# Kernel tuning notes

Measured on AMD Instinct MI355X. Metric: run time of the kernel, lower is better.

Reference implementation:

```python
import jax, jax.numpy as jnp
import numpy as np

N_NODES = 50000
N_EDGES = 800000
NUM_GRAPHS = 512


def gcn_conv(x, edge_index, W, b, num_nodes):
    # PyG GCNConv: h = D^{-1/2} (A + I) D^{-1/2} (x @ W) + b
    h = x @ W
    src, dst = edge_index[0], edge_index[1]
    loop = jnp.arange(num_nodes)
    src = jnp.concatenate([src, loop])
    dst = jnp.concatenate([dst, loop])
    deg = jax.ops.segment_sum(jnp.ones_like(dst, dtype=h.dtype), dst,
                              num_segments=num_nodes)
    dinv = jnp.where(deg > 0, jax.lax.rsqrt(deg), 0.0)
    norm = dinv[src] * dinv[dst]                      # [E+N]
    msg = h[src] * norm[:, None]                      # gather + scale
    out = jax.ops.segment_sum(msg, dst, num_segments=num_nodes)  # scatter-add
    return out + b


def global_mean_pool(x, batch, num_graphs):
    sums = jax.ops.segment_sum(x, batch, num_segments=num_graphs)
    cnts = jax.ops.segment_sum(jnp.ones((x.shape[0],), x.dtype), batch,
                               num_segments=num_graphs)
    return sums / jnp.maximum(cnts, 1.0)[:, None]


def setup_inputs() -> dict:
    key = jax.random.key(0)
    ks = jax.random.split(key, 8)
    x = jax.random.normal(ks[0], (N_NODES, 128), dtype=jnp.float32)
    edge_index = jax.random.randint(ks[1], (2, N_EDGES), 0, N_NODES, dtype=jnp.int64)
    batch = jnp.sort(jax.random.randint(ks[2], (N_NODES,), 0, NUM_GRAPHS, dtype=jnp.int64))
    W1 = jax.random.normal(ks[3], (128, 128), dtype=jnp.float32) * (1.0 / np.sqrt(128))
    b1 = jnp.zeros((128,), jnp.float32)
    W2 = jax.random.normal(ks[4], (128, 64), dtype=jnp.float32) * (1.0 / np.sqrt(128))
    b2 = jnp.zeros((64,), jnp.float32)
    Wl = jax.random.normal(ks[5], (64, 64), dtype=jnp.float32) * (1.0 / np.sqrt(64))
    bl = jnp.zeros((64,), jnp.float32)
    return {"x": x, "edge_index": edge_index, "batch": batch,
            "W1": W1, "b1": b1, "W2": W2, "b2": b2, "Wl": Wl, "bl": bl}


def reference(x, edge_index, batch, W1, b1, W2, b2, Wl, bl):
    num_nodes = x.shape[0]
    h = gcn_conv(x, edge_index, W1, b1, num_nodes)
    h = jax.nn.relu(h)
    h = gcn_conv(h, edge_index, W2, b2, num_nodes)
    g = global_mean_pool(h, batch, NUM_GRAPHS)
    # dropout p=0.5 is identity in eval mode
    return g @ Wl + bl
```

## Files before the change

kernel.cpp:

```cpp
#include <hip/hip_runtime.h>
#include <hip/hip_fp16.h>
#include <math.h>


#define FEAT1 128
#define FEAT2 64
#define BCAP 8192


__global__ void binit_kernel(int* __restrict__ bucket_cursor, int nb) {
    int b = blockIdx.x * 256 + threadIdx.x;
    if (b < nb) bucket_cursor[b] = b * BCAP;
}

__global__ __launch_bounds__(256) void bin_scatter(const int* __restrict__ esrc,
                                                   const int* __restrict__ edst,
                                                   int ne, int nb,
                                                   int* __restrict__ bucket_cursor,
                                                   int* __restrict__ ebin) {
    __shared__ int lcnt[256];
    __shared__ int lcur[256];
    const int tid = threadIdx.x;
    const int e0 = blockIdx.x * 8192;
    lcnt[tid] = 0;
    __syncthreads();
    #pragma unroll 4
    for (int k = 0; k < 32; k++) {
        int e = e0 + k * 256 + tid;
        if (e < ne) atomicAdd(&lcnt[edst[e] >> 8], 1);
    }
    __syncthreads();
    if (tid < nb && lcnt[tid] > 0)
        lcur[tid] = atomicAdd(&bucket_cursor[tid], lcnt[tid]);
    __syncthreads();
    #pragma unroll 4
    for (int k = 0; k < 32; k++) {
        int e = e0 + k * 256 + tid;
        if (e < ne) {
            int d = edst[e];
            int b = d >> 8;
            int p = atomicAdd(&lcur[b], 1);
            if (p < (b + 1) * BCAP)
                ebin[p] = esrc[e] | ((d & 255) << 18);
        }
    }
}

__global__ __launch_bounds__(256) void bucket_csr(const int* __restrict__ ebin,
                                                  const int* __restrict__ bucket_cursor,
                                                  int n_nodes,
                                                  int* __restrict__ csr,
                                                  int2* __restrict__ nodeinfo,
                                                  float* __restrict__ dinv) {
    __shared__ int lcnt[256];
    __shared__ int lscan[256];
    __shared__ int lcur[256];
    const int b = blockIdx.x;
    const int tid = threadIdx.x;
    const int ebeg = b * BCAP;
    int eend = bucket_cursor[b];
    if (eend > ebeg + BCAP) eend = ebeg + BCAP;
    lcnt[tid] = 0;
    __syncthreads();
    for (int e = ebeg + tid; e < eend; e += 256)
        atomicAdd(&lcnt[(ebin[e] >> 18) & 255], 1);
    __syncthreads();
    int v = lcnt[tid];
    lscan[tid] = v;
    __syncthreads();
    for (int off = 1; off < 256; off <<= 1) {
        int u = (tid >= off) ? lscan[tid - off] : 0;
        __syncthreads();
        lscan[tid] += u;
        __syncthreads();
    }
    const int start = ebeg + (lscan[tid] - v);
    const int node = (b << 8) + tid;
    if (node < n_nodes) {
        nodeinfo[node] = make_int2(start, v);
        dinv[node] = (float)(1.0 / sqrt((double)(v + 1)));
    }
    lcur[tid] = start;
    __syncthreads();
    for (int e = ebeg + tid; e < eend; e += 256) {
        int pk = ebin[e];
        int p = atomicAdd(&lcur[(pk >> 18) & 255], 1);
        csr[p] = pk & 0x3FFFF;
    }
}

template <int FOUT>
__global__ __launch_bounds__(256) void gemm_tile_h(const float* __restrict__ A,
                                                   const float* __restrict__ W,
                                                   const float* __restrict__ dinv,
                                                   __half* __restrict__ out, int n) {
    __shared__ float As[64][36];
    __shared__ float Ws[32][68];
    const int tid = threadIdx.x;
    constexpr int NCT = FOUT / 64;
    const int row0 = (blockIdx.x / NCT) * 64;
    const int col0 = (blockIdx.x % NCT) * 64;
    const int rg = tid >> 4;
    const int cg = tid & 15;

    float acc[4][4] = {};

    for (int k0 = 0; k0 < 128; k0 += 32) {
        {
            int r = tid >> 2;
            int k = (tid & 3) * 8;
            int grow = row0 + r;
            float4 v0 = {0.f, 0.f, 0.f, 0.f}, v1 = {0.f, 0.f, 0.f, 0.f};
            if (grow < n) {
                const float* p = A + (size_t)grow * 128 + k0 + k;
                v0 = *(const float4*)(p);
                v1 = *(const float4*)(p + 4);
            }
            *(float4*)(&As[r][k])     = v0;
            *(float4*)(&As[r][k + 4]) = v1;
        }
        {
            int k = tid >> 3;
            int c = (tid & 7) * 8;
            const float* p = W + (size_t)(k0 + k) * FOUT + col0 + c;
            *(float4*)(&Ws[k][c])     = *(const float4*)(p);
            *(float4*)(&Ws[k][c + 4]) = *(const float4*)(p + 4);
        }
        __syncthreads();

        #pragma unroll 8
        for (int k = 0; k < 32; k++) {
            float4 w = *(const float4*)(&Ws[k][cg * 4]);
            float ar0 = As[rg * 4 + 0][k];
            float ar1 = As[rg * 4 + 1][k];
            float ar2 = As[rg * 4 + 2][k];
            float ar3 = As[rg * 4 + 3][k];
            acc[0][0] += ar0 * w.x; acc[0][1] += ar0 * w.y; acc[0][2] += ar0 * w.z; acc[0][3] += ar0 * w.w;
            acc[1][0] += ar1 * w.x; acc[1][1] += ar1 * w.y; acc[1][2] += ar1 * w.z; acc[1][3] += ar1 * w.w;
            acc[2][0] += ar2 * w.x; acc[2][1] += ar2 * w.y; acc[2][2] += ar2 * w.z; acc[2][3] += ar2 * w.w;
            acc[3][0] += ar3 * w.x; acc[3][1] += ar3 * w.y; acc[3][2] += ar3 * w.z; acc[3][3] += ar3 * w.w;
        }
        __syncthreads();
    }

    #pragma unroll
    for (int rr = 0; rr < 4; rr++) {
        int grow = row0 + rg * 4 + rr;
        if (grow < n) {
            float s = dinv[grow];
            __half2 h01 = __floats2half2_rn(acc[rr][0] * s, acc[rr][1] * s);
            __half2 h23 = __floats2half2_rn(acc[rr][2] * s, acc[rr][3] * s);
            __half2* p = (__half2*)(out + (size_t)grow * FOUT + col0 + cg * 4);
            p[0] = h01;
            p[1] = h23;
        }
    }
}

template <int F, bool RELU>
__global__ __launch_bounds__(256) void aggregate_h(const __half* __restrict__ t,
                                                   const float* __restrict__ dinv,
                                                   const int2* __restrict__ nodeinfo,
                                                   const int* __restrict__ csr_src,
                                                   const float* __restrict__ bias,
                                                   float* __restrict__ out, int n) {
    const int wv = threadIdx.x >> 6;
    const int lane = threadIdx.x & 63;
    const int i = blockIdx.x * 4 + wv;
    if (i >= n) return;
    const float di = dinv[i];
    const int2 ni = nodeinfo[i];
    const int e0 = ni.x, e1 = ni.x + ni.y;

    if constexpr (F == 128) {
        float2 a0, a1 = {0.f, 0.f}, a2 = {0.f, 0.f}, a3 = {0.f, 0.f};
        a0 = __half22float2(((const __half2*)(t + (size_t)i * F))[lane]);
        int e = e0;
        for (; e + 4 <= e1; e += 4) {
            int s0 = csr_src[e + 0], s1 = csr_src[e + 1], s2 = csr_src[e + 2], s3 = csr_src[e + 3];
            float2 v0 = __half22float2(((const __half2*)(t + (size_t)s0 * F))[lane]);
            float2 v1 = __half22float2(((const __half2*)(t + (size_t)s1 * F))[lane]);
            float2 v2 = __half22float2(((const __half2*)(t + (size_t)s2 * F))[lane]);
            float2 v3 = __half22float2(((const __half2*)(t + (size_t)s3 * F))[lane]);
            a0.x += v0.x; a0.y += v0.y;
            a1.x += v1.x; a1.y += v1.y;
            a2.x += v2.x; a2.y += v2.y;
            a3.x += v3.x; a3.y += v3.y;
        }
        for (; e < e1; e++) {
            int s = csr_src[e];
            float2 v = __half22float2(((const __half2*)(t + (size_t)s * F))[lane]);
            a0.x += v.x; a0.y += v.y;
        }
        float2 b = ((const float2*)bias)[lane];
        float rx = (a0.x + a1.x + a2.x + a3.x) * di + b.x;
        float ry = (a0.y + a1.y + a2.y + a3.y) * di + b.y;
        if (RELU) { rx = fmaxf(rx, 0.f); ry = fmaxf(ry, 0.f); }
        ((float2*)(out + (size_t)i * F))[lane] = make_float2(rx, ry);
    } else {
        float a0, a1 = 0.f, a2 = 0.f, a3 = 0.f;
        a0 = __half2float(t[(size_t)i * F + lane]);
        int e = e0;
        for (; e + 4 <= e1; e += 4) {
            int s0 = csr_src[e + 0], s1 = csr_src[e + 1], s2 = csr_src[e + 2], s3 = csr_src[e + 3];
            float v0 = __half2float(t[(size_t)s0 * F + lane]);
            float v1 = __half2float(t[(size_t)s1 * F + lane]);
            float v2 = __half2float(t[(size_t)s2 * F + lane]);
            float v3 = __half2float(t[(size_t)s3 * F + lane]);
            a0 += v0; a1 += v1; a2 += v2; a3 += v3;
        }
        for (; e < e1; e++) {
            a0 += __half2float(t[(size_t)csr_src[e] * F + lane]);
        }
        float r = (a0 + a1 + a2 + a3) * di + bias[lane];
        if (RELU) r = fmaxf(r, 0.f);
        out[(size_t)i * F + lane] = r;
    }
}

__global__ __launch_bounds__(256) void pool_classify(const float* __restrict__ h2,
                                                     const int* __restrict__ batch, int n,
                                                     const float* __restrict__ Wl,
                                                     const float* __restrict__ bl,
                                                     float* __restrict__ out) {
    __shared__ float partial[4][64];
    __shared__ float pooled_s[64];
    const int g = blockIdx.x;
    const int wv = threadIdx.x >> 6;
    const int lane = threadIdx.x & 63;

    int lo = 0, hi = n;
    while (lo < hi) { int mid = (lo + hi) >> 1; if (batch[mid] < g) lo = mid + 1; else hi = mid; }
    const int start = lo;
    hi = n;
    while (lo < hi) { int mid = (lo + hi) >> 1; if (batch[mid] < g + 1) lo = mid + 1; else hi = mid; }
    const int end = lo;

    float sum = 0.0f;
    int r = start + wv;
    for (; r + 8 <= end; r += 8) {
        float v0 = h2[(size_t)r * 64 + lane];
        float v1 = h2[(size_t)(r + 4) * 64 + lane];
        sum += v0 + v1;
    }
    for (; r < end; r += 4) sum += h2[(size_t)r * 64 + lane];
    partial[wv][lane] = sum;
    __syncthreads();

    if (wv == 0) {
        float s = partial[0][lane] + partial[1][lane] + partial[2][lane] + partial[3][lane];
        float cnt = (float)(end - start);
        pooled_s[lane] = s / fmaxf(cnt, 1.0f);
    }
    __syncthreads();

    if (wv == 0) {
        float acc = bl[lane];
        #pragma unroll 8
        for (int k = 0; k < 64; k++) acc += pooled_s[k] * Wl[k * 64 + lane];
        out[(size_t)g * 64 + lane] = acc;
    }
}


extern "C" void kernel_launch(void* const* d_in, const int* in_sizes, int n_in,
                              void* d_out, int out_size, void* d_ws, size_t ws_size,
                              hipStream_t stream) {
    const float* x    = (const float*)d_in[0];
    const int*   eidx = (const int*)d_in[1];
    const int*   batch= (const int*)d_in[2];
    const float* W1   = (const float*)d_in[3];
    const float* b1   = (const float*)d_in[4];
    const float* W2   = (const float*)d_in[5];
    const float* b2   = (const float*)d_in[6];
    const float* Wl   = (const float*)d_in[7];
    const float* bl   = (const float*)d_in[8];
    float* out = (float*)d_out;

    const int n_nodes  = in_sizes[0] / FEAT1;
    const int n_edges  = in_sizes[1] / 2;
    const int n_graphs = out_size / FEAT2;
    const int* esrc = eidx;
    const int* edst = eidx + n_edges;
    const int nb = (n_nodes + 255) >> 8;

    char* ws = (char*)d_ws;
    size_t off = 0;
    auto alloc = [&](size_t bytes) -> void* {
        void* p = ws + off;
        off += (bytes + 255) & ~(size_t)255;
        return p;
    };
    __half* t1       = (__half*)alloc((size_t)n_nodes * FEAT1 * 2);
    float*  hb       = (float*)alloc((size_t)n_nodes * FEAT1 * 4);
    float*  dinv     = (float*)alloc((size_t)n_nodes * 4);
    int2*   nodeinfo = (int2*)alloc((size_t)n_nodes * 8);
    int*    bcur     = (int*)alloc((size_t)nb * 4);
    int*    ebin     = (int*)alloc((size_t)nb * BCAP * 4);
    int*    csr      = (int*)alloc((size_t)nb * BCAP * 4);

    binit_kernel<<<(nb + 255) / 256, 256, 0, stream>>>(bcur, nb);
    bin_scatter<<<(n_edges + 8191) / 8192, 256, 0, stream>>>(esrc, edst, n_edges, nb, bcur, ebin);
    bucket_csr<<<nb, 256, 0, stream>>>(ebin, bcur, n_nodes, csr, nodeinfo, dinv);

    gemm_tile_h<FEAT1><<<((n_nodes + 63) / 64) * (FEAT1 / 64), 256, 0, stream>>>(x, W1, dinv, t1, n_nodes);
    aggregate_h<FEAT1, true><<<(n_nodes + 3) / 4, 256, 0, stream>>>(t1, dinv, nodeinfo, csr, b1, hb, n_nodes);

    gemm_tile_h<FEAT2><<<((n_nodes + 63) / 64) * (FEAT2 / 64), 256, 0, stream>>>(hb, W2, dinv, t1, n_nodes);
    aggregate_h<FEAT2, false><<<(n_nodes + 3) / 4, 256, 0, stream>>>(t1, dinv, nodeinfo, csr, b2, hb, n_nodes);

    pool_classify<<<n_graphs, 256, 0, stream>>>(hb, batch, n_nodes, Wl, bl, out);
}
```

Baseline: 181.6 us.

## Use MFMA f16 GEMMs, store hidden layer in fp16, memset bucket cursors

Replaces the scalar FP32 tiled GEMM with a matrix-core kernel using 16x16x32 f16 MFMA. A and W are converted to half in shared memory, and the whole 128-wide K dimension is loaded at once. The first aggregation now writes the ReLU output in fp16, which halves that intermediate's write and the second GEMM's read. Bucket cursors are zeroed with a memset instead of an init kernel and now hold per-bucket relative offsets. The cost is extra rounding from converting the layer-1 activations and weights to fp16, plus a larger shared-memory footprint per block.

Measured after the change: 169.5 us. -6.7%, faster.

```diff
diff --git a/kernel.cpp b/kernel.cpp
--- a/kernel.cpp
+++ b/kernel.cpp
@@ -7,11 +7,10 @@
 #define FEAT2 64
 #define BCAP 8192
 
-
-__global__ void binit_kernel(int* __restrict__ bucket_cursor, int nb) {
-    int b = blockIdx.x * 256 + threadIdx.x;
-    if (b < nb) bucket_cursor[b] = b * BCAP;
-}
+using half8 = __attribute__((ext_vector_type(8))) _Float16;
+using half4 = __attribute__((ext_vector_type(4))) _Float16;
+using f32x4 = __attribute__((ext_vector_type(4))) float;
+
 
 __global__ __launch_bounds__(256) void bin_scatter(const int* __restrict__ esrc,
                                                    const int* __restrict__ edst,
@@ -40,8 +39,8 @@
             int d = edst[e];
             int b = d >> 8;
             int p = atomicAdd(&lcur[b], 1);
-            if (p < (b + 1) * BCAP)
-                ebin[p] = esrc[e] | ((d & 255) << 18);
+            if (p < BCAP)
+                ebin[b * BCAP + p] = esrc[e] | ((d & 255) << 18);
         }
     }
 }
@@ -58,8 +57,9 @@
     const int b = blockIdx.x;
     const int tid = threadIdx.x;
     const int ebeg = b * BCAP;
-    int eend = bucket_cursor[b];
-    if (eend > ebeg + BCAP) eend = ebeg + BCAP;
+    int cnt_b = bucket_cursor[b];
+    if (cnt_b > BCAP) cnt_b = BCAP;
+    const int eend = ebeg + cnt_b;
     lcnt[tid] = 0;
     __syncthreads();
     for (int e = ebeg + tid; e < eend; e += 256)
@@ -89,81 +89,99 @@
     }
 }
 
-template <int FOUT>
-__global__ __launch_bounds__(256) void gemm_tile_h(const float* __restrict__ A,
-                                                   const float* __restrict__ W,
-                                                   const float* __restrict__ dinv,
-                                                   __half* __restrict__ out, int n) {
-    __shared__ float As[64][36];
-    __shared__ float Ws[32][68];
+template <int FOUT, bool A_F16>
+__global__ __launch_bounds__(256) void gemm_mfma(const void* __restrict__ Aptr,
+                                                 const float* __restrict__ W,
+                                                 const float* __restrict__ dinv,
+                                                 _Float16* __restrict__ out, int n) {
+    __shared__ _Float16 As[128 * 136];
+    __shared__ _Float16 Ws[64 * 136];
     const int tid = threadIdx.x;
+    const int wv = tid >> 6;
+    const int lane = tid & 63;
     constexpr int NCT = FOUT / 64;
-    const int row0 = (blockIdx.x / NCT) * 64;
+    const int row0 = (blockIdx.x / NCT) * 128;
     const int col0 = (blockIdx.x % NCT) * 64;
-    const int rg = tid >> 4;
-    const int cg = tid & 15;
-
-    float acc[4][4] = {};
-
-    for (int k0 = 0; k0 < 128; k0 += 32) {
-        {
-            int r = tid >> 2;
-            int k = (tid & 3) * 8;
-            int grow = row0 + r;
-            float4 v0 = {0.f, 0.f, 0.f, 0.f}, v1 = {0.f, 0.f, 0.f, 0.f};
+
+    {
+        const int r = tid >> 1;
+        const int c0 = (tid & 1) * 64;
+        const int grow = row0 + r;
+        if constexpr (A_F16) {
+            const _Float16* A = (const _Float16*)Aptr + (size_t)grow * 128 + c0;
+            #pragma unroll
+            for (int j = 0; j < 8; j++) {
+                half8 v = {};
+                if (grow < n) v = *(const half8*)(A + j * 8);
+                *(half8*)(&As[r * 136 + c0 + j * 8]) = v;
+            }
+        } else {
+            const float* A = (const float*)Aptr + (size_t)grow * 128 + c0;
+            #pragma unroll
+            for (int j = 0; j < 16; j++) {
+                float4 v = {0.f, 0.f, 0.f, 0.f};
+                if (grow < n) v = *(const float4*)(A + j * 4);
+                half4 hv = {(_Float16)v.x, (_Float16)v.y, (_Float16)v.z, (_Float16)v.w};
+                *(half4*)(&As[r * 136 + c0 + j * 4]) = hv;
+            }
+        }
+    }
+    {
+        const int k = tid >> 1;
+        const int cb = (tid & 1) * 32;
+        #pragma unroll
+        for (int j = 0; j < 8; j++) {
+            int c = cb + j * 4;
+            float4 v = *(const float4*)(W + (size_t)k * FOUT + col0 + c);
+            Ws[(c + 0) * 136 + k] = (_Float16)v.x;
+            Ws[(c + 1) * 136 + k] = (_Float16)v.y;
+            Ws[(c + 2) * 136 + k] = (_Float16)v.z;
+            Ws[(c + 3) * 136 + k] = (_Float16)v.w;
+        }
+    }
+    __syncthreads();
+
+    f32x4 acc[2][4] = {};
+    const int mrow = wv * 32 + (lane & 15);
+    const int kb = (lane >> 4) * 8;
+    #pragma unroll
+    for (int ks = 0; ks < 4; ks++) {
+        const int kk = ks * 32 + kb;
+        half8 a0 = *(const half8*)(&As[mrow * 136 + kk]);
+        half8 a1 = *(const half8*)(&As[(mrow + 16) * 136 + kk]);
+        #pragma unroll
+        for (int nj = 0; nj < 4; nj++) {
+            half8 b = *(const half8*)(&Ws[(nj * 16 + (lane & 15)) * 136 + kk]);
+            acc[0][nj] = __builtin_amdgcn_mfma_f32_16x16x32_f16(a0, b, acc[0][nj], 0, 0, 0);
+            acc[1][nj] = __builtin_amdgcn_mfma_f32_16x16x32_f16(a1, b, acc[1][nj], 0, 0, 0);
+        }
+    }
+
+    #pragma unroll
+    for (int mi = 0; mi < 2; mi++) {
+        const int gr0 = row0 + wv * 32 + mi * 16 + (lane >> 4) * 4;
+        #pragma unroll
+        for (int r = 0; r < 4; r++) {
+            const int grow = gr0 + r;
             if (grow < n) {
-                const float* p = A + (size_t)grow * 128 + k0 + k;
-                v0 = *(const float4*)(p);
-                v1 = *(const float4*)(p + 4);
+                const float s = dinv[grow];
+                #pragma unroll
+                for (int nj = 0; nj < 4; nj++) {
+                    out[(size_t)grow * FOUT + col0 + nj * 16 + (lane & 15)] =
+                        (_Float16)(acc[mi][nj][r] * s);
+                }
             }
-            *(float4*)(&As[r][k])     = v0;
-            *(float4*)(&As[r][k + 4]) = v1;
-        }
-        {
-            int k = tid >> 3;
-            int c = (tid & 7) * 8;
-            const float* p = W + (size_t)(k0 + k) * FOUT + col0 + c;
-            *(float4*)(&Ws[k][c])     = *(const float4*)(p);
-            *(float4*)(&Ws[k][c + 4]) = *(const float4*)(p + 4);
-        }
-        __syncthreads();
-
-        #pragma unroll 8
-        for (int k = 0; k < 32; k++) {
-            float4 w = *(const float4*)(&Ws[k][cg * 4]);
-            float ar0 = As[rg * 4 + 0][k];
-            float ar1 = As[rg * 4 + 1][k];
-            float ar2 = As[rg * 4 + 2][k];
-            float ar3 = As[rg * 4 + 3][k];
-            acc[0][0] += ar0 * w.x; acc[0][1] += ar0 * w.y; acc[0][2] += ar0 * w.z; acc[0][3] += ar0 * w.w;
-            acc[1][0] += ar1 * w.x; acc[1][1] += ar1 * w.y; acc[1][2] += ar1 * w.z; acc[1][3] += ar1 * w.w;
-            acc[2][0] += ar2 * w.x; acc[2][1] += ar2 * w.y; acc[2][2] += ar2 * w.z; acc[2][3] += ar2 * w.w;
-            acc[3][0] += ar3 * w.x; acc[3][1] += ar3 * w.y; acc[3][2] += ar3 * w.z; acc[3][3] += ar3 * w.w;
-        }
-        __syncthreads();
-    }
-
-    #pragma unroll
-    for (int rr = 0; rr < 4; rr++) {
-        int grow = row0 + rg * 4 + rr;
-        if (grow < n) {
-            float s = dinv[grow];
-            __half2 h01 = __floats2half2_rn(acc[rr][0] * s, acc[rr][1] * s);
-            __half2 h23 = __floats2half2_rn(acc[rr][2] * s, acc[rr][3] * s);
-            __half2* p = (__half2*)(out + (size_t)grow * FOUT + col0 + cg * 4);
-            p[0] = h01;
-            p[1] = h23;
-        }
-    }
-}
-
-template <int F, bool RELU>
+        }
+    }
+}
+
+template <int F, bool RELU, bool OUT16>
 __global__ __launch_bounds__(256) void aggregate_h(const __half* __restrict__ t,
                                                    const float* __restrict__ dinv,
                                                    const int2* __restrict__ nodeinfo,
                                                    const int* __restrict__ csr_src,
                                                    const float* __restrict__ bias,
-                                                   float* __restrict__ out, int n) {
+                                                   void* __restrict__ outp, int n) {
     const int wv = threadIdx.x >> 6;
     const int lane = threadIdx.x & 63;
     const int i = blockIdx.x * 4 + wv;
@@ -196,7 +214,11 @@
         float rx = (a0.x + a1.x + a2.x + a3.x) * di + b.x;
         float ry = (a0.y + a1.y + a2.y + a3.y) * di + b.y;
         if (RELU) { rx = fmaxf(rx, 0.f); ry = fmaxf(ry, 0.f); }
-        ((float2*)(out + (size_t)i * F))[lane] = make_float2(rx, ry);
+        if constexpr (OUT16) {
+            ((__half2*)((__half*)outp + (size_t)i * F))[lane] = __floats2half2_rn(rx, ry);
+        } else {
+            ((float2*)((float*)outp + (size_t)i * F))[lane] = make_float2(rx, ry);
+        }
     } else {
         float a0, a1 = 0.f, a2 = 0.f, a3 = 0.f;
         a0 = __half2float(t[(size_t)i * F + lane]);
@@ -214,7 +236,11 @@
         }
         float r = (a0 + a1 + a2 + a3) * di + bias[lane];
         if (RELU) r = fmaxf(r, 0.f);
-        out[(size_t)i * F + lane] = r;
+        if constexpr (OUT16) {
+            ((__half*)outp)[(size_t)i * F + lane] = __float2half(r);
+        } else {
+            ((float*)outp)[(size_t)i * F + lane] = r;
+        }
     }
 }
 
@@ -291,23 +317,28 @@
         off += (bytes + 255) & ~(size_t)255;
         return p;
     };
-    __half* t1       = (__half*)alloc((size_t)n_nodes * FEAT1 * 2);
-    float*  hb       = (float*)alloc((size_t)n_nodes * FEAT1 * 4);
-    float*  dinv     = (float*)alloc((size_t)n_nodes * 4);
+    _Float16* t1     = (_Float16*)alloc((size_t)n_nodes * FEAT1 * 2);
+    __half*   h1h    = (__half*)alloc((size_t)n_nodes * FEAT1 * 2);
+    float*    h2     = (float*)alloc((size_t)n_nodes * FEAT2 * 4);
+    float*    dinv   = (float*)alloc((size_t)n_nodes * 4);
     int2*   nodeinfo = (int2*)alloc((size_t)n_nodes * 8);
     int*    bcur     = (int*)alloc((size_t)nb * 4);
     int*    ebin     = (int*)alloc((size_t)nb * BCAP * 4);
     int*    csr      = (int*)alloc((size_t)nb * BCAP * 4);
 
-    binit_kernel<<<(nb + 255) / 256, 256, 0, stream>>>(bcur, nb);
+    const int nrb = (n_nodes + 127) / 128;
+
+    hipMemsetAsync(bcur, 0, (size_t)nb * 4, stream);
     bin_scatter<<<(n_edges + 8191) / 8192, 256, 0, stream>>>(esrc, edst, n_edges, nb, bcur, ebin);
     bucket_csr<<<nb, 256, 0, stream>>>(ebin, bcur, n_nodes, csr, nodeinfo, dinv);
 
-    gemm_tile_h<FEAT1><<<((n_nodes + 63) / 64) * (FEAT1 / 64), 256, 0, stream>>>(x, W1, dinv, t1, n_nodes);
-    aggregate_h<FEAT1, true><<<(n_nodes + 3) / 4, 256, 0, stream>>>(t1, dinv, nodeinfo, csr, b1, hb, n_nodes);
-
-    gemm_tile_h<FEAT2><<<((n_nodes + 63) / 64) * (FEAT2 / 64), 256, 0, stream>>>(hb, W2, dinv, t1, n_nodes);
-    aggregate_h<FEAT2, false><<<(n_nodes + 3) / 4, 256, 0, stream>>>(t1, dinv, nodeinfo, csr, b2, hb, n_nodes);
-
-    pool_classify<<<n_graphs, 256, 0, stream>>>(hb, batch, n_nodes, Wl, bl, out);
-}
+    gemm_mfma<FEAT1, false><<<nrb * (FEAT1 / 64), 256, 0, stream>>>(x, W1, dinv, t1, n_nodes);
+    aggregate_h<FEAT1, true, true><<<(n_nodes + 3) / 4, 256, 0, stream>>>(
+        (const __half*)t1, dinv, nodeinfo, csr, b1, h1h, n_nodes);
+
+    gemm_mfma<FEAT2, true><<<nrb * (FEAT2 / 64), 256, 0, stream>>>(h1h, W2, dinv, t1, n_nodes);
+    aggregate_h<FEAT2, false, false><<<(n_nodes + 3) / 4, 256, 0, stream>>>(
+        (const __half*)t1, dinv, nodeinfo, csr, b2, h2, n_nodes);
+
+    pool_classify<<<n_graphs, 256, 0, stream>>>(h2, batch, n_nodes, Wl, bl, out);
+}
```
